# Kernel tuning notes

Measured on AMD Instinct MI355X. Metric: run time of the kernel, lower is better.

The kernel has to match this reference:

```python
import jax, jax.numpy as jnp
import numpy as np

WINDOW = (7, 7)
SHIFT = (3, 3)
NUM_HEADS = 4
DIM = 128


def _rel_pos_index():
    wh, ww = WINDOW
    coords = np.stack(np.meshgrid(np.arange(wh), np.arange(ww), indexing='ij'))  # [2,wh,ww]
    cf = coords.reshape(2, -1)                    # [2, N]
    rc = (cf[:, :, None] - cf[:, None, :]).transpose(1, 2, 0)  # [N,N,2]
    rc[:, :, 0] += wh - 1
    rc[:, :, 1] += ww - 1
    rc[:, :, 0] *= 2 * ww - 1
    return jnp.asarray(rc.sum(-1).reshape(-1))    # [N*N] int


def _attn_mask_np(pH, pW, sh):
    # Static-shape shift mask (host-side numpy; constant under jit).
    wh, ww = WINDOW
    m = np.zeros((pH, pW))
    h_slices = ((0, pH - wh), (pH - wh, pH - sh[0]), (pH - sh[0], pH))
    w_slices = ((0, pW - ww), (pW - ww, pW - sh[1]), (pW - sh[1], pW))
    cnt = 0
    for hs in h_slices:
        for ws in w_slices:
            m[hs[0]:hs[1], ws[0]:ws[1]] = cnt
            cnt += 1
    m = m.reshape(pH // wh, wh, pW // ww, ww).transpose(0, 2, 1, 3).reshape(-1, wh * ww)
    diff = m[:, None, :] - m[:, :, None]          # [num_windows, N, N]
    return jnp.asarray(np.where(diff != 0, -100.0, 0.0), dtype=np.float32)


def setup_inputs() -> dict:
    key = jax.random.key(0)
    ks = jax.random.split(key, 9)
    B, H, W, C = 32, 56, 56, DIM
    return {
        'input_q': jax.random.normal(ks[0], (B, H, W, C), jnp.float32),
        'input_k': jax.random.normal(ks[1], (B, H, W, C), jnp.float32),
        'input_v': jax.random.normal(ks[2], (B, H, W, C), jnp.float32),
        'q_weight': jax.random.normal(ks[3], (C, C), jnp.float32) * 0.05,
        'q_bias': jnp.zeros((C,), jnp.float32),
        'k_weight': jax.random.normal(ks[4], (C, C), jnp.float32) * 0.05,
        'k_bias': jnp.zeros((C,), jnp.float32),
        'v_weight': jax.random.normal(ks[5], (C, C), jnp.float32) * 0.05,
        'v_bias': jnp.zeros((C,), jnp.float32),
        'proj_weight': jax.random.normal(ks[6], (C, C), jnp.float32) * 0.05,
        'proj_bias': jnp.zeros((C,), jnp.float32),
        'rpb_table': jax.random.normal(ks[7], ((2 * WINDOW[0] - 1) * (2 * WINDOW[1] - 1), NUM_HEADS), jnp.float32) * 0.02,
    }


def reference(input_q, input_k, input_v, q_weight, q_bias, k_weight, k_bias,
              v_weight, v_bias, proj_weight, proj_bias, rpb_table):
    B, H, W, C = input_q.shape
    wh, ww = WINDOW
    pad_b = (wh - H % wh) % wh
    pad_r = (ww - W % ww) % ww
    pad = lambda t: jnp.pad(t, ((0, 0), (0, pad_b), (0, pad_r), (0, 0)))
    qx, kx, vx = pad(input_q), pad(input_k), pad(input_v)
    pad_H, pad_W = H + pad_b, W + pad_r
    sh = [0 if wh >= pad_H else SHIFT[0], 0 if ww >= pad_W else SHIFT[1]]
    if sum(sh) > 0:
        roll = lambda t: jnp.roll(t, (-sh[0], -sh[1]), axis=(1, 2))
        qx, kx, vx = roll(qx), roll(kx), roll(vx)
    nWh, nWw = pad_H // wh, pad_W // ww
    num_windows = nWh * nWw
    N = wh * ww

    def part(t):  # [B,pH,pW,C] -> [B*num_windows, N, C]
        t = t.reshape(B, nWh, wh, nWw, ww, C).transpose(0, 1, 3, 2, 4, 5)
        return t.reshape(B * num_windows, N, C)

    qx, kx, vx = part(qx), part(kx), part(vx)
    hd = C // NUM_HEADS

    def heads(x, w, b):  # linear + split heads -> [BW, nH, N, hd]
        return (x @ w.T + b).reshape(-1, N, NUM_HEADS, hd).transpose(0, 2, 1, 3)

    q = heads(qx, q_weight, q_bias) * (hd ** -0.5)
    k = heads(kx, k_weight, k_bias)
    v = heads(vx, v_weight, v_bias)

    attn = jnp.einsum('whqd,whkd->whqk', q, k)    # [BW, nH, N, N]
    rpb = rpb_table[_rel_pos_index()].reshape(N, N, NUM_HEADS).transpose(2, 0, 1)[None]
    attn = attn + rpb
    if sum(sh) > 0:
        mask = _attn_mask_np(pad_H, pad_W, sh)    # [num_windows, N, N]
        attn = attn.reshape(B, num_windows, NUM_HEADS, N, N) + mask[None, :, None]
        attn = attn.reshape(B * num_windows, NUM_HEADS, N, N)
    attn = jax.nn.softmax(attn, axis=-1)

    x = jnp.einsum('whqk,whkd->whqd', attn, v).transpose(0, 2, 1, 3).reshape(B * num_windows, N, C)
    x = x @ proj_weight.T + proj_bias
    x = x.reshape(B, nWh, nWw, wh, ww, C).transpose(0, 1, 3, 2, 4, 5).reshape(B, pad_H, pad_W, C)
    if sum(sh) > 0:
        x = jnp.roll(x, (sh[0], sh[1]), axis=(1, 2))
    return x[:, :H, :W, :]
```

## Files before the change

kernel.cpp:

```cpp
#include <hip/hip_runtime.h>
#include <hip/hip_bf16.h>

typedef __attribute__((ext_vector_type(8))) short s16x8;
typedef __attribute__((ext_vector_type(4))) float f32x4;
typedef __attribute__((ext_vector_type(2))) unsigned int u32x2;
typedef __attribute__((ext_vector_type(4))) unsigned int u32x4;

#define MFMA16(a, b, c) __builtin_amdgcn_mfma_f32_16x16x32_bf16((a), (b), (c), 0, 0, 0)
#define LOG2E 1.4426950408889634f

#define ROR16(x, CTRL) \
  __int_as_float(__builtin_amdgcn_update_dpp(0, __float_as_int(x), (CTRL), 0xF, 0xF, true))

static __device__ __forceinline__ unsigned int pk2(float a, float b) {
  union { __hip_bfloat162 h2; unsigned int u; } cv;
  cv.h2 = __float22bfloat162_rn(make_float2(a, b));
  return cv.u;
}
static __device__ __forceinline__ int div7(int x) { return (x * 9363) >> 16; }
static __device__ __forceinline__ int swz256(int row, int byteoff) {
  return row * 256 + (byteoff ^ ((row & 7) << 4));
}
static __device__ __forceinline__ int swz128(int row, int byteoff) {
  return row * 128 + (byteoff ^ ((row & 7) << 4));
}

__global__ void swin_prep(const float* __restrict__ wq, const float* __restrict__ wk,
                          const float* __restrict__ wv, const float* __restrict__ wp,
                          const float* __restrict__ rpb_table,
                          unsigned short* __restrict__ wsW, float* __restrict__ rpbm) {
  int idx = blockIdx.x * 256 + threadIdx.x;
  if (idx < 65536) {
    int t = idx >> 14, loc = idx & 16383;
    const float* s = (t == 0) ? wq : (t == 1) ? wk : (t == 2) ? wv : wp;
    union { __hip_bfloat16 h; unsigned short u; } cv;
    cv.h = __float2bfloat16(s[loc]);
    wsW[idx] = cv.u;
  } else {
    int k = idx - 65536;
    int c = k >> 14;
    int h = (k >> 12) & 3;
    int i = (k >> 6) & 63, j = k & 63;
    float val;
    if (j >= 49) val = -1e30f;
    else if (i >= 49) val = 0.f;
    else {
      int yi = div7(i), xi = i - yi * 7;
      int yj = div7(j), xj = j - yj * 7;
      int ridx = (yi - yj + 6) * 13 + (xi - xj + 6);
      val = rpb_table[ridx * 4 + h];
      int cwi = c >> 1, cwj = c & 1;
      int rgi = (cwi ? (yi < 4 ? 3 : 6) : 0) + (cwj ? (xi < 4 ? 1 : 2) : 0);
      int rgj = (cwi ? (yj < 4 ? 3 : 6) : 0) + (cwj ? (xj < 4 ? 1 : 2) : 0);
      if (rgi != rgj) val -= 100.f;
      val *= LOG2E;
    }
    rpbm[k] = val;
  }
}

__global__ __launch_bounds__(512, 4) void swin_main(
    const float* __restrict__ xq, const float* __restrict__ xk, const float* __restrict__ xv,
    const float* __restrict__ bq, const float* __restrict__ bk, const float* __restrict__ bv,
    const float* __restrict__ bp, const unsigned short* __restrict__ wsW,
    const float* __restrict__ rpbm, float* __restrict__ out) {
  __shared__ __align__(16) char sm[65536];

  const int tid = threadIdx.x;
  const int lane = tid & 63;
  const int wv_ = tid >> 6;
  const int l15 = lane & 15;
  const int lg = lane >> 4;
  const int kgrp = lg * 8;
  const int rsub = lg * 4;

  const int bid = blockIdx.x;
  const int b = bid >> 6;
  const int widx = bid & 63;
  const int wi = widx >> 3, wj = widx & 7;
  const long obase = (long)b * 56 * 56 * 128;
  const int mcase = ((wi == 7) ? 2 : 0) + ((wj == 7) ? 1 : 0);

  const int h = wv_ & 3;
  const int half = wv_ >> 2;
  const int coff = h * 32;

  const int xrow = tid >> 3;
  const int xk16 = (tid & 7) << 4;
  long xoff = -1;
  if (xrow < 49) {
    int ty = div7(xrow), tx = xrow - ty * 7;
    int ih = wi * 7 + ty + 3; if (ih >= 56) ih -= 56;
    int iw = wj * 7 + tx + 3; if (iw >= 56) iw -= 56;
    xoff = obase + (long)((ih * 56 + iw) * 128 + xk16);
  }

  auto issue_x = [&](const float* src, float* r) {
#pragma unroll
    for (int i = 0; i < 16; ++i) r[i] = 0.f;
    if (xoff >= 0) {
      const float* p = src + xoff;
#pragma unroll
      for (int q = 0; q < 4; ++q) {
        f32x4 v = *(const f32x4*)(p + q * 4);
        r[q * 4 + 0] = v[0]; r[q * 4 + 1] = v[1];
        r[q * 4 + 2] = v[2]; r[q * 4 + 3] = v[3];
      }
    }
  };
  auto write_x = [&](int base, const float* r) {
    unsigned int w[8];
#pragma unroll
    for (int i = 0; i < 8; ++i) w[i] = pk2(r[2 * i], r[2 * i + 1]);
    u32x4 a = {w[0], w[1], w[2], w[3]};
    u32x4 bb = {w[4], w[5], w[6], w[7]};
    *(u32x4*)(sm + base + swz256(xrow, xk16 * 2)) = a;
    *(u32x4*)(sm + base + swz256(xrow, xk16 * 2 + 16)) = bb;
  };
  auto st2 = [&](int a0, int a1, float v0, float v1) {
    unsigned int u = pk2(v0, v1);
    *(unsigned short*)(sm + a0) = (unsigned short)u;
    *(unsigned short*)(sm + a1) = (unsigned short)(u >> 16);
  };

  float xra[16], xrb[16];
  issue_x(xq, xra);
  issue_x(xk, xrb);

  f32x4 rvv[2][4];
  {
    const float* rpbm_h = rpbm + (((mcase << 2) + h) << 12);
#pragma unroll
    for (int m2 = 0; m2 < 2; ++m2)
#pragma unroll
      for (int r = 0; r < 4; ++r) {
        int i = (half * 2 + m2) * 16 + rsub + r;
        const float* rp = rpbm_h + i * 64 + l15;
#pragma unroll
        for (int jt = 0; jt < 4; ++jt) rvv[m2][jt][r] = rp[jt * 16];
      }
  }

  auto linearT = [&](int woff, const float* bias, float scale, int srcbase, int dstbase) {
    const int nrow = wv_ * 16 + l15;
    s16x8 afr[4];
#pragma unroll
    for (int kt = 0; kt < 4; ++kt)
      afr[kt] = *(const s16x8*)(wsW + woff + nrow * 128 + kt * 32 + kgrp);
    f32x4 bv4 = *(const f32x4*)(bias + wv_ * 16 + rsub);
    float bb0 = bv4[0] * scale, bb1 = bv4[1] * scale;
    float bb2 = bv4[2] * scale, bb3 = bv4[3] * scale;
    __builtin_amdgcn_s_setprio(1);
#pragma unroll
    for (int tt = 0; tt < 4; ++tt) {
      f32x4 acc = {0.f, 0.f, 0.f, 0.f};
#pragma unroll
      for (int kt = 0; kt < 4; ++kt) {
        s16x8 bfr = *(const s16x8*)(sm + srcbase + swz256(tt * 16 + l15, (kt * 32 + kgrp) * 2));
        acc = MFMA16(afr[kt], bfr, acc);
      }
      u32x2 pkw = {pk2(acc[0] * scale + bb0, acc[1] * scale + bb1),
                   pk2(acc[2] * scale + bb2, acc[3] * scale + bb3)};
      *(u32x2*)(sm + dstbase + swz256(tt * 16 + l15, 2 * (wv_ * 16 + rsub))) = pkw;
    }
    __builtin_amdgcn_s_setprio(0);
  };

  auto linearV = [&](int woff, const float* bias) {
    const int n = wv_ * 16 + l15;
    s16x8 bfr[4];
#pragma unroll
    for (int kt = 0; kt < 4; ++kt)
      bfr[kt] = *(const s16x8*)(wsW + woff + n * 128 + kt * 32 + kgrp);
    float bval = bias[n];
    __builtin_amdgcn_s_setprio(1);
#pragma unroll
    for (int mt = 0; mt < 4; ++mt) {
      f32x4 acc = {0.f, 0.f, 0.f, 0.f};
#pragma unroll
      for (int kt = 0; kt < 4; ++kt) {
        s16x8 afr = *(const s16x8*)(sm + swz256(mt * 16 + l15, (kt * 32 + kgrp) * 2));
        acc = MFMA16(afr, bfr[kt], acc);
      }
      u32x2 pkw = {pk2(acc[0] + bval, acc[1] + bval), pk2(acc[2] + bval, acc[3] + bval)};
      *(u32x2*)(sm + 49152 + swz128(n, 2 * (mt * 16 + rsub))) = pkw;
    }
    __builtin_amdgcn_s_setprio(0);
  };

  const float QSCALE = 0.17677669529663687f * LOG2E;

  write_x(0, xra);
  write_x(49152, xrb);
  __syncthreads();

  issue_x(xv, xra);
  linearT(0, bq, QSCALE, 0, 16384);
  __syncthreads();

  write_x(0, xra);
  linearT(16384, bk, 1.f, 49152, 32768);
  __syncthreads();

  f32x4 S[2][4];
  {
    linearV(32768, bv);

    s16x8 kfr[4];
#pragma unroll
    for (int jt = 0; jt < 4; ++jt)
      kfr[jt] = *(const s16x8*)(sm + 32768 + swz256(jt * 16 + l15, (coff + kgrp) * 2));
    __builtin_amdgcn_s_setprio(1);
#pragma unroll
    for (int m2 = 0; m2 < 2; ++m2) {
      int mt = half * 2 + m2;
      s16x8 qfr = *(const s16x8*)(sm + 16384 + swz256(mt * 16 + l15, (coff + kgrp) * 2));
#pragma unroll
      for (int jt = 0; jt < 4; ++jt)
        S[m2][jt] = MFMA16(qfr, kfr[jt], rvv[m2][jt]);
    }
    __builtin_amdgcn_s_setprio(0);

#pragma unroll
    for (int m2 = 0; m2 < 2; ++m2) {
#pragma unroll
      for (int r = 0; r < 4; ++r) {
        float m = fmaxf(fmaxf(S[m2][0][r], S[m2][1][r]), fmaxf(S[m2][2][r], S[m2][3][r]));
        m = fmaxf(m, ROR16(m, 0x128));
        m = fmaxf(m, ROR16(m, 0x124));
        m = fmaxf(m, ROR16(m, 0x122));
        m = fmaxf(m, ROR16(m, 0x121));
        float e0 = __builtin_amdgcn_exp2f(S[m2][0][r] - m);
        float e1 = __builtin_amdgcn_exp2f(S[m2][1][r] - m);
        float e2 = __builtin_amdgcn_exp2f(S[m2][2][r] - m);
        float e3 = __builtin_amdgcn_exp2f(S[m2][3][r] - m);
        float s = e0 + e1 + e2 + e3;
        s += ROR16(s, 0x128);
        s += ROR16(s, 0x124);
        s += ROR16(s, 0x122);
        s += ROR16(s, 0x121);
        float inv = 1.0f / s;
        S[m2][0][r] = e0 * inv; S[m2][1][r] = e1 * inv;
        S[m2][2][r] = e2 * inv; S[m2][3][r] = e3 * inv;
      }
    }
  }
  __syncthreads();

  const int pbase = 16384 + h * 8192;
#pragma unroll
  for (int m2 = 0; m2 < 2; ++m2) {
    int i0 = (half * 2 + m2) * 16 + rsub;
#pragma unroll
    for (int jt = 0; jt < 4; ++jt) {
      int bo = 2 * (jt * 16 + l15);
      st2(pbase + swz128(i0, bo), pbase + swz128(i0 + 1, bo), S[m2][jt][0], S[m2][jt][1]);
      st2(pbase + swz128(i0 + 2, bo), pbase + swz128(i0 + 3, bo), S[m2][jt][2], S[m2][jt][3]);
    }
  }
  {
    s16x8 vfr[2][2];
#pragma unroll
    for (int ks = 0; ks < 2; ++ks)
#pragma unroll
      for (int ct = 0; ct < 2; ++ct) {
        int c = coff + ct * 16 + l15;
        vfr[ks][ct] = *(const s16x8*)(sm + 49152 + swz128(c, (ks * 32 + kgrp) * 2));
      }
    f32x4 Oacc[2][2];
#pragma unroll
    for (int ct = 0; ct < 2; ++ct)
#pragma unroll
      for (int qt = 0; qt < 2; ++qt) Oacc[ct][qt] = (f32x4){0.f, 0.f, 0.f, 0.f};
    __builtin_amdgcn_s_setprio(1);
#pragma unroll
    for (int qt = 0; qt < 2; ++qt) {
#pragma unroll
      for (int ks = 0; ks < 2; ++ks) {
        s16x8 pfr = *(const s16x8*)(sm + pbase + swz128((half * 2 + qt) * 16 + l15, (ks * 32 + kgrp) * 2));
        Oacc[0][qt] = MFMA16(vfr[ks][0], pfr, Oacc[0][qt]);
        Oacc[1][qt] = MFMA16(vfr[ks][1], pfr, Oacc[1][qt]);
      }
    }
    __builtin_amdgcn_s_setprio(0);
#pragma unroll
    for (int ct = 0; ct < 2; ++ct)
#pragma unroll
      for (int qt = 0; qt < 2; ++qt) {
        int qtok = (half * 2 + qt) * 16 + l15;
        u32x2 pkw = {pk2(Oacc[ct][qt][0], Oacc[ct][qt][1]),
                     pk2(Oacc[ct][qt][2], Oacc[ct][qt][3])};
        *(u32x2*)(sm + swz256(qtok, 2 * (coff + ct * 16 + rsub))) = pkw;
      }
  }
  __syncthreads();

  {
    const int nrow = wv_ * 16 + l15;
    s16x8 afr[4];
#pragma unroll
    for (int kt = 0; kt < 4; ++kt)
      afr[kt] = *(const s16x8*)(wsW + 49152 + nrow * 128 + kt * 32 + kgrp);
    f32x4 bv4 = *(const f32x4*)(bp + wv_ * 16 + rsub);
    __builtin_amdgcn_s_setprio(1);
#pragma unroll
    for (int tt = 0; tt < 4; ++tt) {
      f32x4 acc = {0.f, 0.f, 0.f, 0.f};
#pragma unroll
      for (int kt = 0; kt < 4; ++kt) {
        s16x8 bfr = *(const s16x8*)(sm + swz256(tt * 16 + l15, (kt * 32 + kgrp) * 2));
        acc = MFMA16(afr[kt], bfr, acc);
      }
      int tok = tt * 16 + l15;
      if (tok < 49) {
        int ty = div7(tok), tx = tok - ty * 7;
        int oh = wi * 7 + ty + 3; if (oh >= 56) oh -= 56;
        int ow = wj * 7 + tx + 3; if (ow >= 56) ow -= 56;
        f32x4 res = {acc[0] + bv4[0], acc[1] + bv4[1], acc[2] + bv4[2], acc[3] + bv4[3]};
        *(f32x4*)(out + obase + (oh * 56 + ow) * 128 + wv_ * 16 + rsub) = res;
      }
    }
    __builtin_amdgcn_s_setprio(0);
  }
}

extern "C" void kernel_launch(void* const* d_in, const int* in_sizes, int n_in,
                              void* d_out, int out_size, void* d_ws, size_t ws_size,
                              hipStream_t stream) {
  const float* xq = (const float*)d_in[0];
  const float* xk = (const float*)d_in[1];
  const float* xv = (const float*)d_in[2];
  const float* wq = (const float*)d_in[3];
  const float* bq = (const float*)d_in[4];
  const float* wk = (const float*)d_in[5];
  const float* bk = (const float*)d_in[6];
  const float* wv = (const float*)d_in[7];
  const float* bv = (const float*)d_in[8];
  const float* wp = (const float*)d_in[9];
  const float* bp = (const float*)d_in[10];
  const float* rpb = (const float*)d_in[11];

  unsigned short* wsW = (unsigned short*)d_ws;
  float* rpbm = (float*)((char*)d_ws + 131072);

  swin_prep<<<512, 256, 0, stream>>>(wq, wk, wv, wp, rpb, wsW, rpbm);

  float* out = (float*)d_out;
  swin_main<<<2048, 512, 0, stream>>>(xq, xk, xv, bq, bk, bv, bp, wsW, rpbm, out);
}
```

Before: 76.01 us.

## Fold weight conversion and bias-mask table build into main kernel, drop prep launch

Removes the separate prep kernel that converted weights to bf16 and precomputed the relative-position-bias plus shift-mask table. The main kernel now loads fp32 weights directly and packs them to bf16 in registers. It also computes each bias/mask value on the fly from the small rpb table and the window region indices. This saves one kernel launch and its workspace traffic, at the cost of twice the weight bytes per block and extra integer arithmetic plus scattered table gathers in every one of the 2048 blocks.

```diff
diff --git a/kernel.cpp b/kernel.cpp
--- a/kernel.cpp
+++ b/kernel.cpp
@@ -24,46 +24,21 @@
 static __device__ __forceinline__ int swz128(int row, int byteoff) {
   return row * 128 + (byteoff ^ ((row & 7) << 4));
 }
-
-__global__ void swin_prep(const float* __restrict__ wq, const float* __restrict__ wk,
-                          const float* __restrict__ wv, const float* __restrict__ wp,
-                          const float* __restrict__ rpb_table,
-                          unsigned short* __restrict__ wsW, float* __restrict__ rpbm) {
-  int idx = blockIdx.x * 256 + threadIdx.x;
-  if (idx < 65536) {
-    int t = idx >> 14, loc = idx & 16383;
-    const float* s = (t == 0) ? wq : (t == 1) ? wk : (t == 2) ? wv : wp;
-    union { __hip_bfloat16 h; unsigned short u; } cv;
-    cv.h = __float2bfloat16(s[loc]);
-    wsW[idx] = cv.u;
-  } else {
-    int k = idx - 65536;
-    int c = k >> 14;
-    int h = (k >> 12) & 3;
-    int i = (k >> 6) & 63, j = k & 63;
-    float val;
-    if (j >= 49) val = -1e30f;
-    else if (i >= 49) val = 0.f;
-    else {
-      int yi = div7(i), xi = i - yi * 7;
-      int yj = div7(j), xj = j - yj * 7;
-      int ridx = (yi - yj + 6) * 13 + (xi - xj + 6);
-      val = rpb_table[ridx * 4 + h];
-      int cwi = c >> 1, cwj = c & 1;
-      int rgi = (cwi ? (yi < 4 ? 3 : 6) : 0) + (cwj ? (xi < 4 ? 1 : 2) : 0);
-      int rgj = (cwi ? (yj < 4 ? 3 : 6) : 0) + (cwj ? (xj < 4 ? 1 : 2) : 0);
-      if (rgi != rgj) val -= 100.f;
-      val *= LOG2E;
-    }
-    rpbm[k] = val;
-  }
+static __device__ __forceinline__ s16x8 ldw8(const float* p) {
+  f32x4 a = *(const f32x4*)p;
+  f32x4 b = *(const f32x4*)(p + 4);
+  union { u32x4 u; s16x8 s; } cv;
+  cv.u = (u32x4){pk2(a[0], a[1]), pk2(a[2], a[3]), pk2(b[0], b[1]), pk2(b[2], b[3])};
+  return cv.s;
 }
 
 __global__ __launch_bounds__(512, 4) void swin_main(
     const float* __restrict__ xq, const float* __restrict__ xk, const float* __restrict__ xv,
-    const float* __restrict__ bq, const float* __restrict__ bk, const float* __restrict__ bv,
-    const float* __restrict__ bp, const unsigned short* __restrict__ wsW,
-    const float* __restrict__ rpbm, float* __restrict__ out) {
+    const float* __restrict__ wq, const float* __restrict__ bq,
+    const float* __restrict__ wk, const float* __restrict__ bk,
+    const float* __restrict__ wv, const float* __restrict__ bv,
+    const float* __restrict__ wp, const float* __restrict__ bp,
+    const float* __restrict__ rpb_table, float* __restrict__ out) {
   __shared__ __align__(16) char sm[65536];
 
   const int tid = threadIdx.x;
@@ -79,7 +54,6 @@
   const int widx = bid & 63;
   const int wi = widx >> 3, wj = widx & 7;
   const long obase = (long)b * 56 * 56 * 128;
-  const int mcase = ((wi == 7) ? 2 : 0) + ((wj == 7) ? 1 : 0);
 
   const int h = wv_ & 3;
   const int half = wv_ >> 2;
@@ -129,24 +103,52 @@
 
   f32x4 rvv[2][4];
   {
-    const float* rpbm_h = rpbm + (((mcase << 2) + h) << 12);
+    const int cwi = (wi == 7), cwj = (wj == 7);
+    int jj[4], rgj[4]; bool jv[4];
+#pragma unroll
+    for (int jt = 0; jt < 4; ++jt) {
+      int j = jt * 16 + l15;
+      jv[jt] = (j < 49);
+      int jc = jv[jt] ? j : 0;
+      int yj = div7(jc), xj = jc - yj * 7;
+      jj[jt] = yj * 13 + xj;
+      rgj[jt] = (cwi ? (yj < 4 ? 3 : 6) : 0) + (cwj ? (xj < 4 ? 1 : 2) : 0);
+    }
 #pragma unroll
     for (int m2 = 0; m2 < 2; ++m2)
 #pragma unroll
       for (int r = 0; r < 4; ++r) {
         int i = (half * 2 + m2) * 16 + rsub + r;
-        const float* rp = rpbm_h + i * 64 + l15;
-#pragma unroll
-        for (int jt = 0; jt < 4; ++jt) rvv[m2][jt][r] = rp[jt * 16];
-      }
-  }
-
-  auto linearT = [&](int woff, const float* bias, float scale, int srcbase, int dstbase) {
+        if (i < 49) {
+          int yi = div7(i), xi = i - yi * 7;
+          int ri = yi * 13 + xi + 84;
+          int rgi = (cwi ? (yi < 4 ? 3 : 6) : 0) + (cwj ? (xi < 4 ? 1 : 2) : 0);
+#pragma unroll
+          for (int jt = 0; jt < 4; ++jt) {
+            float v;
+            if (jv[jt]) {
+              v = rpb_table[(ri - jj[jt]) * 4 + h];
+              if (rgi != rgj[jt]) v -= 100.f;
+              v *= LOG2E;
+            } else {
+              v = -1e30f;
+            }
+            rvv[m2][jt][r] = v;
+          }
+        } else {
+#pragma unroll
+          for (int jt = 0; jt < 4; ++jt)
+            rvv[m2][jt][r] = jv[jt] ? 0.f : -1e30f;
+        }
+      }
+  }
+
+  auto linearT = [&](const float* w, const float* bias, float scale, int srcbase, int dstbase) {
     const int nrow = wv_ * 16 + l15;
     s16x8 afr[4];
 #pragma unroll
     for (int kt = 0; kt < 4; ++kt)
-      afr[kt] = *(const s16x8*)(wsW + woff + nrow * 128 + kt * 32 + kgrp);
+      afr[kt] = ldw8(w + nrow * 128 + kt * 32 + kgrp);
     f32x4 bv4 = *(const f32x4*)(bias + wv_ * 16 + rsub);
     float bb0 = bv4[0] * scale, bb1 = bv4[1] * scale;
     float bb2 = bv4[2] * scale, bb3 = bv4[3] * scale;
@@ -166,12 +168,12 @@
     __builtin_amdgcn_s_setprio(0);
   };
 
-  auto linearV = [&](int woff, const float* bias) {
+  auto linearV = [&](const float* w, const float* bias) {
     const int n = wv_ * 16 + l15;
     s16x8 bfr[4];
 #pragma unroll
     for (int kt = 0; kt < 4; ++kt)
-      bfr[kt] = *(const s16x8*)(wsW + woff + n * 128 + kt * 32 + kgrp);
+      bfr[kt] = ldw8(w + n * 128 + kt * 32 + kgrp);
     float bval = bias[n];
     __builtin_amdgcn_s_setprio(1);
 #pragma unroll
@@ -195,16 +197,16 @@
   __syncthreads();
 
   issue_x(xv, xra);
-  linearT(0, bq, QSCALE, 0, 16384);
+  linearT(wq, bq, QSCALE, 0, 16384);
   __syncthreads();
 
   write_x(0, xra);
-  linearT(16384, bk, 1.f, 49152, 32768);
+  linearT(wk, bk, 1.f, 49152, 32768);
   __syncthreads();
 
   f32x4 S[2][4];
   {
-    linearV(32768, bv);
+    linearV(wv, bv);
 
     s16x8 kfr[4];
 #pragma unroll
@@ -300,7 +302,7 @@
     s16x8 afr[4];
 #pragma unroll
     for (int kt = 0; kt < 4; ++kt)
-      afr[kt] = *(const s16x8*)(wsW + 49152 + nrow * 128 + kt * 32 + kgrp);
+      afr[kt] = ldw8(wp + nrow * 128 + kt * 32 + kgrp);
     f32x4 bv4 = *(const f32x4*)(bp + wv_ * 16 + rsub);
     __builtin_amdgcn_s_setprio(1);
 #pragma unroll
@@ -340,11 +342,6 @@
   const float* bp = (const float*)d_in[10];
   const float* rpb = (const float*)d_in[11];
 
-  unsigned short* wsW = (unsigned short*)d_ws;
-  float* rpbm = (float*)((char*)d_ws + 131072);
-
-  swin_prep<<<512, 256, 0, stream>>>(wq, wk, wv, wp, rpb, wsW, rpbm);
-
   float* out = (float*)d_out;
-  swin_main<<<2048, 512, 0, stream>>>(xq, xk, xv, bq, bk, bv, bp, wsW, rpbm, out);
-}
+  swin_main<<<2048, 512, 0, stream>>>(xq, xk, xv, wq, bq, wk, bk, wv, bv, wp, bp, rpb, out);
+}
```

After: 115.5 us. 52.0% more time.
